# Kernel optimization log

Hardware: AMD Instinct MI355X
Metric: run time of the kernel (lower is better)

## Reference

```python
import jax, jax.numpy as jnp
import numpy as np

MAX_LAB = 64  # cap on connected-component ids per sample (original cc3d is unbounded)
BIG = jnp.int32(2 ** 30)


def _cc_label(mask):
    """26-connectivity connected components of a 3D bool mask via label propagation.
    Each component ends with label == max initial voxel id in it (nonzero), bg = 0."""
    n = mask.size
    init = jnp.where(mask, jnp.arange(1, n + 1, dtype=jnp.int32).reshape(mask.shape), jnp.int32(0))

    def cond(st):
        return jnp.any(st[0] != st[1])

    def body(st):
        lab = st[0]
        # max over 3x3x3 neighborhood == 26-connectivity propagation step
        neigh = jax.lax.reduce_window(lab, jnp.int32(0), jax.lax.max, (3, 3, 3), (1, 1, 1), 'SAME')
        return (jnp.where(mask, neigh, jnp.int32(0)), lab)

    lab, _ = jax.lax.while_loop(cond, body, (init, jnp.full_like(init, -1)))
    return lab


def _compact(lab):
    """Relabel a per-sample label map to consecutive ids 0,1..k (0 = background),
    matching cc3d's 1..k numbering."""
    u = jnp.unique(lab, size=MAX_LAB + 1, fill_value=BIG)  # sorted: [0, l1, .., lk, BIG..]
    return jnp.searchsorted(u, lab).astype(jnp.int32)


def _instance_dice(x, y):
    xb = jnp.squeeze(x, 1) > 0.5  # [B,D,H,W] pred foreground
    yb = jnp.squeeze(y, 1) > 0.5  # [B,D,H,W] gt foreground
    label = jax.vmap(lambda m: _compact(_cc_label(m)))
    gt_lab = label(yb)  # per-sample ids 0..k_i (ids shared across batch, as in original)
    pr_lab = label(xb)
    M = MAX_LAB + 1
    # joint histogram over (gt component id, pred component id), global across batch
    idx = gt_lab.reshape(-1) * M + pr_lab.reshape(-1)
    overlap = jax.ops.segment_sum(jnp.ones(idx.shape, jnp.float32), idx, num_segments=M * M).reshape(M, M)
    gt_size = overlap.sum(1)  # [M] voxels per gt id
    pr_size = overlap.sum(0)  # [M] voxels per pred id
    ov = overlap[1:, 1:]                       # [G,P] fg-fg overlaps
    inter_mask = ov > 0                        # pred comp p intersects gt comp g
    inter = ov.sum(1)                          # [G] |gt_g  ∩  union(intersecting preds)|
    union_sz = (inter_mask * pr_size[1:]).sum(1)  # [G] |union of intersecting pred comps|
    has_inter = inter > 0
    dice = jnp.where(has_inter, 2.0 * inter / jnp.maximum(union_sz + gt_size[1:], 1.0), 0.0)
    lesion_dice = dice.sum()
    num_gt = jnp.sum(gt_size[1:] > 0).astype(jnp.float32)
    tp_mask = inter_mask.any(0)                # [P] pred comps matched to some gt
    num_fp = jnp.sum((pr_size[1:] > 0) & ~tp_mask).astype(jnp.float32)
    return lesion_dice / (num_gt + num_fp)


def setup_inputs() -> dict:
    B, D, H, W = 2, 128, 128, 128
    R, N_BLOBS = 5, 12
    rng = np.random.default_rng(0)
    zz, yy, xx = np.meshgrid(np.arange(D), np.arange(H), np.arange(W), indexing='ij')

    def blobs(k):
        m = np.zeros((B, D, H, W), bool)
        for b in range(B):
            c = rng.integers(R + 2, D - R - 2, size=(k, 3))
            for cz, cy, cx in c:
                m[b] |= (zz - cz) ** 2 + (yy - cy) ** 2 + (xx - cx) ** 2 <= R * R
        return m

    y = blobs(N_BLOBS)
    # prediction = slightly shifted gt (partial-overlap TPs) + extra false-positive blobs
    x = np.roll(y, shift=(2, 1, 0), axis=(1, 2, 3)) | blobs(4)
    return {"x": jnp.asarray(x[:, None].astype(np.float32)),
            "y": jnp.asarray(y[:, None].astype(np.float32))}


def reference(x, y):
    return _instance_dice(x, y)
```

## Files before the change

kernel.cpp:

```cpp
#include <hip/hip_runtime.h>


#define NVOX (128 * 128 * 128)
#define NTOT (2 * NVOX)
#define NBLK 4096
#define CAP 12288
#define ML 65
#define NSLAB 8
#define ZSLAB 16
#define EDGE_CAP 8192
#define OVBLK 48

__global__ __launch_bounds__(256) void k_count(
    const float4* __restrict__ x, const float4* __restrict__ y,
    unsigned char* __restrict__ maskArr, int* __restrict__ blkCnt,
    int* __restrict__ overlap, int* __restrict__ cnt) {
    int t = blockIdx.x * 256 + threadIdx.x;
    float4 xv = x[t];
    float4 yv = y[t];
    unsigned m = 0;
    if (xv.x > 0.5f) m |= 1u;
    if (xv.y > 0.5f) m |= 2u;
    if (xv.z > 0.5f) m |= 4u;
    if (xv.w > 0.5f) m |= 8u;
    if (yv.x > 0.5f) m |= 16u;
    if (yv.y > 0.5f) m |= 32u;
    if (yv.z > 0.5f) m |= 64u;
    if (yv.w > 0.5f) m |= 128u;
    maskArr[t] = (unsigned char)m;
    int v = __popc(m & 0xFu) | (__popc(m >> 4) << 16);
    #pragma unroll
    for (int d = 1; d < 64; d <<= 1) v += __shfl_xor(v, d);
    __shared__ int ws[4];
    if ((threadIdx.x & 63) == 0) ws[threadIdx.x >> 6] = v;
    __syncthreads();
    if (threadIdx.x == 0) blkCnt[blockIdx.x] = ws[0] + ws[1] + ws[2] + ws[3];
    if (blockIdx.x == 0) {
        for (int i = threadIdx.x; i < ML * ML; i += 256) overlap[i] = 0;
        if (threadIdx.x < 8) cnt[8 + threadIdx.x] = 0;
    }
}

__global__ __launch_bounds__(1024) void k_scan(
    const int* __restrict__ blkCnt, int* __restrict__ blkOff, int* __restrict__ cnt) {
    int t = threadIdx.x;
    int base = t * 4;
    int a0 = blkCnt[base], a1 = blkCnt[base + 1], a2 = blkCnt[base + 2], a3 = blkCnt[base + 3];
    int s = a0 + a1 + a2 + a3;
    int lane = t & 63, wave = t >> 6;
    int v = s;
    #pragma unroll
    for (int d = 1; d < 64; d <<= 1) {
        int u = __shfl_up(v, d);
        if (lane >= d) v += u;
    }
    __shared__ int wsum[16];
    __shared__ int segb;
    if (lane == 63) wsum[wave] = v;
    __syncthreads();
    int woff = 0;
    for (int k = 0; k < wave; ++k) woff += wsum[k];
    int incl = v + woff;
    int excl = incl - s;
    if (t == 511) segb = incl;
    __syncthreads();
    int sub = (base >= 2048) ? segb : 0;
    int e0 = excl - sub;
    blkOff[base]     = e0;
    blkOff[base + 1] = e0 + a0;
    blkOff[base + 2] = e0 + a0 + a1;
    blkOff[base + 3] = e0 + a0 + a1 + a2;
    if (t == 511) { cnt[0] = incl & 0xFFFF; cnt[2] = incl >> 16; }
    if (t == 1023) {
        cnt[1] = (incl & 0xFFFF) - (segb & 0xFFFF);
        cnt[3] = (incl >> 16)    - (segb >> 16);
    }
}

__global__ __launch_bounds__(256) void k_fill(
    const unsigned char* __restrict__ maskArr, const int* __restrict__ blkOff,
    unsigned short* __restrict__ posMapX, unsigned short* __restrict__ posMapY,
    int* __restrict__ lists) {
    int blk = blockIdx.x;
    int t = blk * 256 + threadIdx.x;
    int b = blk >> 11;
    unsigned m = maskArr[t];
    int px = __popc(m & 0xFu), py = __popc(m >> 4);
    int pk = px | (py << 16);
    int lane = threadIdx.x & 63, wave = threadIdx.x >> 6;
    int v = pk;
    #pragma unroll
    for (int d = 1; d < 64; d <<= 1) {
        int u = __shfl_up(v, d);
        if (lane >= d) v += u;
    }
    __shared__ int wsum[4];
    if (lane == 63) wsum[wave] = v;
    __syncthreads();
    int woff = 0;
    for (int k = 0; k < wave; ++k) woff += wsum[k];
    int incl = v + woff;
    int off = blkOff[blk];
    int baseX = (off & 0xFFFF) + (incl & 0xFFFF) - px;
    int baseY = (off >> 16)    + (incl >> 16)    - py;
    int i = t << 2;
    int j = i & (NVOX - 1);
    ushort4 pxv, pyv;
    unsigned short* ppx = &pxv.x;
    unsigned short* ppy = &pyv.x;
    int cx = 0, cy = 0;
    #pragma unroll
    for (int k = 0; k < 4; ++k) {
        unsigned short vx = 0, vy = 0;
        if (m & (1u << k)) {
            int pos = baseX + cx++;
            if (pos < CAP) { lists[(0 + b) * CAP + pos] = j + k; vx = (unsigned short)(pos + 1); }
        }
        if (m & (1u << (k + 4))) {
            int pos = baseY + cy++;
            if (pos < CAP) { lists[(2 + b) * CAP + pos] = j + k; vy = (unsigned short)(pos + 1); }
        }
        ppx[k] = vx;
        ppy[k] = vy;
    }
    ((ushort4*)posMapX)[t] = pxv;
    ((ushort4*)posMapY)[t] = pyv;
}

__device__ __forceinline__ int find_root(volatile unsigned* parent, int i) {
    unsigned p = parent[i];
    while (p != (unsigned)i) {
        unsigned gp = parent[p];
        if (gp != p) parent[i] = gp;
        i = (int)p;
        p = gp;
    }
    return i;
}

__device__ __forceinline__ void lds_union(unsigned* parentNV, int a, int b) {
    volatile unsigned* parent = (volatile unsigned*)parentNV;
    int ra = find_root(parent, a);
    int rb = find_root(parent, b);
    while (ra != rb) {
        int lo = ra < rb ? ra : rb;
        int hi = ra < rb ? rb : ra;
        unsigned old = atomicCAS(&parentNV[lo], (unsigned)lo, (unsigned)hi);
        if (old == (unsigned)lo) return;
        ra = find_root(parent, (int)old);
        rb = find_root(parent, hi);
    }
}

__global__ __launch_bounds__(1024) void k_cc_local(
    const unsigned short* __restrict__ posMapX, const unsigned short* __restrict__ posMapY,
    const int* __restrict__ lists, const int* __restrict__ blkOff,
    int* __restrict__ cnt, int* __restrict__ rootPos, int* __restrict__ edges) {
    int fb = blockIdx.y;
    int slab = blockIdx.x;
    int f = fb >> 1, b = fb & 1;
    const unsigned short* posMap = (f ? posMapY : posMapX) + (b << 21);
    const int* fgl = lists + fb * CAP;
    int n = cnt[fb]; if (n > CAP) n = CAP;
    int blkbase = b * 2048 + slab * 256;
    int o0 = blkOff[blkbase];
    int s0 = f ? (o0 >> 16) : (o0 & 0xFFFF);
    int s1;
    if (slab == NSLAB - 1) s1 = n;
    else { int o1 = blkOff[blkbase + 256]; s1 = f ? (o1 >> 16) : (o1 & 0xFFFF); }
    if (s1 > n) s1 = n;
    int ns = s1 - s0;
    if (ns <= 0) return;

    __shared__ unsigned parent[CAP];
    int tid = threadIdx.x;
    int lane = tid & 63;
    int iters = (ns + 1023) >> 10;

    for (int it = 0; it < iters; ++it) {
        int q = it * 1024 + tid;
        if (q < ns) {
            int p = s0 + q;
            int j = fgl[p];
            unsigned par = (unsigned)q;
            if (p + 1 < s1 && (j & 127) != 127) {
                if (fgl[p + 1] == j + 1) par = (unsigned)(q + 1);
            }
            parent[q] = par;
        }
    }
    __syncthreads();

    for (int it = 0; it < iters; ++it) {
        int q = it * 1024 + tid;
        bool active = q < ns;
        int j = active ? fgl[s0 + q] : 0;
        int z = j >> 14, y = (j >> 7) & 127, x0 = j & 127;
        bool ztop = ((z & (ZSLAB - 1)) == (ZSLAB - 1));
        unsigned short qv[12];
        int idx = 0;
        #pragma unroll
        for (int dx = -1; dx <= 1; ++dx) {
            int yy = y + 1, xx = x0 + dx;
            bool ok = active && yy <= 127 && (unsigned)xx <= 127u;
            int nj = (z << 14) + (yy << 7) + xx;
            qv[idx++] = ok ? posMap[nj] : (unsigned short)0;
        }
        #pragma unroll
        for (int dy = -1; dy <= 1; ++dy)
            #pragma unroll
            for (int dx = -1; dx <= 1; ++dx) {
                int zz = z + 1, yy = y + dy, xx = x0 + dx;
                bool ok = active && zz <= 127 && (unsigned)yy <= 127u && (unsigned)xx <= 127u;
                int nj = (zz << 14) + (yy << 7) + xx;
                qv[idx++] = ok ? posMap[nj] : (unsigned short)0;
            }
        #pragma unroll
        for (int k = 0; k < 3; ++k)
            if (qv[k]) lds_union(parent, q, (int)qv[k] - 1 - s0);
        if (!ztop) {
            #pragma unroll
            for (int k = 3; k < 12; ++k)
                if (qv[k]) lds_union(parent, q, (int)qv[k] - 1 - s0);
        }
        int ec = 0;
        int myE[9];
        if (ztop) {
            #pragma unroll
            for (int k = 3; k < 12; ++k)
                if (qv[k]) myE[ec++] = (s0 + q) | (((int)qv[k] - 1) << 14);
        }
        int pref = ec;
        #pragma unroll
        for (int d = 1; d < 64; d <<= 1) {
            int u = __shfl_up(pref, d);
            if (lane >= d) pref += u;
        }
        int total = __shfl(pref, 63);
        if (total > 0) {
            int base = 0;
            if (lane == 63) base = atomicAdd(cnt + 8 + fb, total);
            base = __shfl(base, 63);
            int o = base + pref - ec;
            for (int k = 0; k < ec; ++k)
                if (o + k < EDGE_CAP) edges[fb * EDGE_CAP + o + k] = myE[k];
        }
    }
    __syncthreads();

    for (int it = 0; it < iters; ++it) {
        int q = it * 1024 + tid;
        if (q < ns)
            rootPos[fb * CAP + s0 + q] = s0 + find_root((volatile unsigned*)parent, q);
    }
}

__device__ __forceinline__ int rank_of(const int* sortedL, int nr, int v) {
    int lo = 0, hi = nr;
    while (lo < hi) { int mid = (lo + hi) >> 1; if (sortedL[mid] < v) lo = mid + 1; else hi = mid; }
    return lo;
}

__global__ __launch_bounds__(1024) void k_cc_merge(
    const int* __restrict__ cnt, const int* __restrict__ rootPos,
    const int* __restrict__ edges, unsigned char* __restrict__ lab8) {
    int fb = blockIdx.x;
    int tid = threadIdx.x;
    int n = cnt[fb]; if (n > CAP) n = CAP;
    int ne = cnt[8 + fb]; if (ne > EDGE_CAP) ne = EDGE_CAP;

    __shared__ unsigned parent[CAP];
    __shared__ int slabRoots[1024];
    __shared__ int rootsL[128];
    __shared__ int sortedL[64];
    __shared__ int nsrSh, nrSh;

    if (tid == 0) { nsrSh = 0; nrSh = 0; }
    __syncthreads();
    for (int p = tid; p < n; p += 1024) {
        unsigned r = (unsigned)rootPos[fb * CAP + p];
        parent[p] = r;
        if (r == (unsigned)p) {
            int s = atomicAdd(&nsrSh, 1);
            if (s < 1024) slabRoots[s] = p;
        }
    }
    __syncthreads();

    for (int e = tid; e < ne; e += 1024) {
        int pk = edges[fb * EDGE_CAP + e];
        lds_union(parent, pk & 0x3FFF, pk >> 14);
    }
    __syncthreads();

    int nsr = nsrSh; if (nsr > 1024) nsr = 1024;
    for (int i = tid; i < nsr; i += 1024) {
        int r = slabRoots[i];
        if (parent[r] == (unsigned)r) {
            int s = atomicAdd(&nrSh, 1);
            if (s < 128) rootsL[s] = r;
        }
    }
    __syncthreads();
    int nr = nrSh; if (nr > 64) nr = 64;
    if (tid < nr) {
        int v = rootsL[tid];
        int r = 0;
        for (int k = 0; k < nr; ++k) r += (rootsL[k] < v) ? 1 : 0;
        sortedL[r] = v;
    }
    __syncthreads();

    for (int i = tid; i < nsr; i += 1024) {
        int r = slabRoots[i];
        int fr = find_root((volatile unsigned*)parent, r);
        lab8[fb * CAP + r] = (unsigned char)(1 + rank_of(sortedL, nr, fr));
    }
}

__device__ __forceinline__ void hist_add_pred(int* ovl, int key, bool valid) {
    unsigned long long remaining = __ballot(valid ? 1 : 0);
    int lane = threadIdx.x & 63;
    while (remaining) {
        int leader = __ffsll(remaining) - 1;
        int lkey = __shfl(key, leader);
        unsigned long long m = __ballot((valid && lkey == key) ? 1 : 0) & remaining;
        if (lane == leader) atomicAdd(&ovl[lkey], (int)__popcll(m));
        remaining &= ~m;
    }
}

__global__ __launch_bounds__(256) void k_overlap_final(
    const unsigned short* __restrict__ posMapX, const unsigned short* __restrict__ posMapY,
    const int* __restrict__ lists, int* __restrict__ cnt,
    const int* __restrict__ rootPos, const unsigned char* __restrict__ lab8,
    int* __restrict__ overlap, float* __restrict__ out) {
    int fb = blockIdx.y;
    int f = fb >> 1, b = fb & 1;
    int n = cnt[fb]; if (n > CAP) n = CAP;
    int t = blockIdx.x * 256 + threadIdx.x;
    bool valid = t < n;
    int key = 0;
    if (valid) {
        int j = lists[fb * CAP + t];
        int gi = (b << 21) + j;
        if (f == 0) {
            int pc = (int)lab8[fb * CAP + rootPos[fb * CAP + t]];
            int q = (int)posMapY[gi];
            int gc = 0;
            if (q) gc = (int)lab8[(2 + b) * CAP + rootPos[(2 + b) * CAP + (q - 1)]];
            key = gc * ML + pc;
        } else {
            if (posMapX[gi] != 0) valid = false;
            else {
                int gc = (int)lab8[fb * CAP + rootPos[fb * CAP + t]];
                key = gc * ML;
            }
        }
    }
    hist_add_pred(overlap, key, valid);

    __shared__ int lastFlag;
    __syncthreads();
    if (threadIdx.x == 0) {
        __threadfence();
        lastFlag = (atomicAdd(&cnt[12], 1) == 4 * OVBLK - 1) ? 1 : 0;
    }
    __syncthreads();
    if (!lastFlag) return;

    __shared__ int O[ML * ML];
    __shared__ float prs[ML];
    __shared__ unsigned char tp[ML];
    __shared__ float diceSh[ML];
    __shared__ int ngSh[ML];
    __shared__ int nfSh[ML];
    int tid = threadIdx.x;
    for (int i = tid; i < ML * ML; i += 256) O[i] = overlap[i];
    __syncthreads();
    if (tid < ML) {
        int s = 0; int any = 0;
        for (int g = 0; g < ML; ++g) {
            int o = O[g * ML + tid];
            s += o;
            if (g >= 1 && o > 0) any = 1;
        }
        prs[tid] = (float)s;
        tp[tid] = (unsigned char)any;
    }
    __syncthreads();
    if (tid < ML) {
        float dice = 0.f; int ng = 0, nf = 0;
        if (tid >= 1) {
            int gt = 0, inter = 0; float un = 0.f;
            for (int p = 0; p < ML; ++p) {
                int o = O[tid * ML + p];
                gt += o;
                if (p >= 1) { inter += o; if (o > 0) un += prs[p]; }
            }
            if (inter > 0) {
                float den = un + (float)gt;
                if (den < 1.f) den = 1.f;
                dice = 2.f * (float)inter / den;
            }
            ng = (gt > 0) ? 1 : 0;
            nf = (prs[tid] > 0.f && tp[tid] == 0) ? 1 : 0;
        }
        diceSh[tid] = dice; ngSh[tid] = ng; nfSh[tid] = nf;
    }
    __syncthreads();
    if (tid == 0) {
        float ld = 0.f; int ng = 0, nf = 0;
        for (int k = 1; k < ML; ++k) { ld += diceSh[k]; ng += ngSh[k]; nf += nfSh[k]; }
        out[0] = ld / (float)(ng + nf);
    }
}

extern "C" void kernel_launch(void* const* d_in, const int* in_sizes, int n_in,
                              void* d_out, int out_size, void* d_ws, size_t ws_size,
                              hipStream_t stream) {
    const float* x = (const float*)d_in[0];
    const float* y = (const float*)d_in[1];
    float* out = (float*)d_out;

    char* base = (char*)d_ws;
    int* cnt            = (int*)base;
    int* overlap        = cnt + 16;
    int* blkCnt         = overlap + ML * ML;
    int* blkOff         = blkCnt + NBLK;
    int* lists          = blkOff + NBLK;
    int* rootPos        = lists + 4 * CAP;
    int* edges          = rootPos + 4 * CAP;
    unsigned char* lab8 = (unsigned char*)(edges + 4 * EDGE_CAP);
    unsigned char* maskArr = lab8 + 4 * CAP;
    size_t off = (size_t)((maskArr + NTOT / 4) - (unsigned char*)base);
    off = (off + 15) & ~(size_t)15;
    unsigned short* posMapX = (unsigned short*)(base + off);
    unsigned short* posMapY = posMapX + NTOT;

    k_count<<<NBLK, 256, 0, stream>>>((const float4*)x, (const float4*)y,
                                      maskArr, blkCnt, overlap, cnt);
    k_scan<<<1, 1024, 0, stream>>>(blkCnt, blkOff, cnt);
    k_fill<<<NBLK, 256, 0, stream>>>(maskArr, blkOff, posMapX, posMapY, lists);
    k_cc_local<<<dim3(NSLAB, 4), 1024, 0, stream>>>(posMapX, posMapY, lists,
                                                    blkOff, cnt, rootPos, edges);
    k_cc_merge<<<4, 1024, 0, stream>>>(cnt, rootPos, edges, lab8);
    k_overlap_final<<<dim3(OVBLK, 4), 256, 0, stream>>>(
        posMapX, posMapY, lists, cnt, rootPos, lab8, overlap, out);
}
```

Baseline: 142.9 us.

## Fold block scan into fill and merge CC stage via last-block pattern

Removes the single-block scan kernel: every fill block now reads all 4096 block counts and computes its own prefix offset and the per-sample totals redundantly. The local connected-components kernel and the merge kernel are fused, with the last slab block per (field, batch) pair detected through an atomic counter plus threadfence and then doing the merge. This cuts two kernel launches and their serialization gaps. In exchange every fill block reads 16 KB of counts, and the merge now runs on only the last-arriving block while sharing LDS with the local stage.

```diff
diff --git a/kernel.cpp b/kernel.cpp
--- a/kernel.cpp
+++ b/kernel.cpp
@@ -37,72 +37,75 @@
     if (threadIdx.x == 0) blkCnt[blockIdx.x] = ws[0] + ws[1] + ws[2] + ws[3];
     if (blockIdx.x == 0) {
         for (int i = threadIdx.x; i < ML * ML; i += 256) overlap[i] = 0;
-        if (threadIdx.x < 8) cnt[8 + threadIdx.x] = 0;
-    }
-}
-
-__global__ __launch_bounds__(1024) void k_scan(
-    const int* __restrict__ blkCnt, int* __restrict__ blkOff, int* __restrict__ cnt) {
-    int t = threadIdx.x;
-    int base = t * 4;
-    int a0 = blkCnt[base], a1 = blkCnt[base + 1], a2 = blkCnt[base + 2], a3 = blkCnt[base + 3];
-    int s = a0 + a1 + a2 + a3;
-    int lane = t & 63, wave = t >> 6;
-    int v = s;
+        if (threadIdx.x < 16) cnt[8 + threadIdx.x] = 0;
+    }
+}
+
+__global__ __launch_bounds__(256) void k_fill(
+    const unsigned char* __restrict__ maskArr, const int* __restrict__ blkCnt,
+    int* __restrict__ blkOff, int* __restrict__ cnt,
+    unsigned short* __restrict__ posMapX, unsigned short* __restrict__ posMapY,
+    int* __restrict__ lists) {
+    int blk = blockIdx.x;
+    int tid = threadIdx.x;
+    int lane = tid & 63, wave = tid >> 6;
+
+    int A = 0, B = 0, C = 0;
+    #pragma unroll
+    for (int k = 0; k < 4; ++k) {
+        int4 c4 = ((const int4*)blkCnt)[tid * 4 + k];
+        int i0 = tid * 16 + k * 4;
+        const int* cc = &c4.x;
+        #pragma unroll
+        for (int j = 0; j < 4; ++j) {
+            int c = cc[j];
+            int i = i0 + j;
+            C += c;
+            if (i < 2048) B += c;
+            if (i < blk)  A += c;
+        }
+    }
+    #pragma unroll
+    for (int d = 1; d < 64; d <<= 1) {
+        A += __shfl_xor(A, d);
+        B += __shfl_xor(B, d);
+        C += __shfl_xor(C, d);
+    }
+    __shared__ int rA[4], rB[4], rC[4];
+    if (lane == 0) { rA[wave] = A; rB[wave] = B; rC[wave] = C; }
+    __syncthreads();
+    A = rA[0] + rA[1] + rA[2] + rA[3];
+    B = rB[0] + rB[1] + rB[2] + rB[3];
+    C = rC[0] + rC[1] + rC[2] + rC[3];
+    int base = A - (blk >= 2048 ? B : 0);
+    if (tid == 0) {
+        blkOff[blk] = base;
+        if (blk == 0) {
+            cnt[0] = B & 0xFFFF;
+            cnt[2] = B >> 16;
+            cnt[1] = (C & 0xFFFF) - (B & 0xFFFF);
+            cnt[3] = (C >> 16)    - (B >> 16);
+        }
+    }
+
+    int t = blk * 256 + tid;
+    int b = blk >> 11;
+    unsigned m = maskArr[t];
+    int px = __popc(m & 0xFu), py = __popc(m >> 4);
+    int v = px | (py << 16);
     #pragma unroll
     for (int d = 1; d < 64; d <<= 1) {
         int u = __shfl_up(v, d);
         if (lane >= d) v += u;
     }
-    __shared__ int wsum[16];
-    __shared__ int segb;
+    __shared__ int wsum[4];
     if (lane == 63) wsum[wave] = v;
     __syncthreads();
     int woff = 0;
     for (int k = 0; k < wave; ++k) woff += wsum[k];
     int incl = v + woff;
-    int excl = incl - s;
-    if (t == 511) segb = incl;
-    __syncthreads();
-    int sub = (base >= 2048) ? segb : 0;
-    int e0 = excl - sub;
-    blkOff[base]     = e0;
-    blkOff[base + 1] = e0 + a0;
-    blkOff[base + 2] = e0 + a0 + a1;
-    blkOff[base + 3] = e0 + a0 + a1 + a2;
-    if (t == 511) { cnt[0] = incl & 0xFFFF; cnt[2] = incl >> 16; }
-    if (t == 1023) {
-        cnt[1] = (incl & 0xFFFF) - (segb & 0xFFFF);
-        cnt[3] = (incl >> 16)    - (segb >> 16);
-    }
-}
-
-__global__ __launch_bounds__(256) void k_fill(
-    const unsigned char* __restrict__ maskArr, const int* __restrict__ blkOff,
-    unsigned short* __restrict__ posMapX, unsigned short* __restrict__ posMapY,
-    int* __restrict__ lists) {
-    int blk = blockIdx.x;
-    int t = blk * 256 + threadIdx.x;
-    int b = blk >> 11;
-    unsigned m = maskArr[t];
-    int px = __popc(m & 0xFu), py = __popc(m >> 4);
-    int pk = px | (py << 16);
-    int lane = threadIdx.x & 63, wave = threadIdx.x >> 6;
-    int v = pk;
-    #pragma unroll
-    for (int d = 1; d < 64; d <<= 1) {
-        int u = __shfl_up(v, d);
-        if (lane >= d) v += u;
-    }
-    __shared__ int wsum[4];
-    if (lane == 63) wsum[wave] = v;
-    __syncthreads();
-    int woff = 0;
-    for (int k = 0; k < wave; ++k) woff += wsum[k];
-    int incl = v + woff;
-    int off = blkOff[blk];
-    int baseX = (off & 0xFFFF) + (incl & 0xFFFF) - px;
-    int baseY = (off >> 16)    + (incl >> 16)    - py;
+    int baseX = (base & 0xFFFF) + (incl & 0xFFFF) - px;
+    int baseY = (base >> 16)    + (incl >> 16)    - py;
     int i = t << 2;
     int j = i & (NVOX - 1);
     ushort4 pxv, pyv;
@@ -152,10 +155,17 @@
     }
 }
 
-__global__ __launch_bounds__(1024) void k_cc_local(
+__device__ __forceinline__ int rank_of(const int* sortedL, int nr, int v) {
+    int lo = 0, hi = nr;
+    while (lo < hi) { int mid = (lo + hi) >> 1; if (sortedL[mid] < v) lo = mid + 1; else hi = mid; }
+    return lo;
+}
+
+__global__ __launch_bounds__(1024) void k_cc(
     const unsigned short* __restrict__ posMapX, const unsigned short* __restrict__ posMapY,
     const int* __restrict__ lists, const int* __restrict__ blkOff,
-    int* __restrict__ cnt, int* __restrict__ rootPos, int* __restrict__ edges) {
+    int* __restrict__ cnt, int* __restrict__ rootPos, int* __restrict__ edges,
+    unsigned char* __restrict__ lab8) {
     int fb = blockIdx.y;
     int slab = blockIdx.x;
     int f = fb >> 1, b = fb & 1;
@@ -170,113 +180,109 @@
     else { int o1 = blkOff[blkbase + 256]; s1 = f ? (o1 >> 16) : (o1 & 0xFFFF); }
     if (s1 > n) s1 = n;
     int ns = s1 - s0;
-    if (ns <= 0) return;
-
-    __shared__ unsigned parent[CAP];
-    int tid = threadIdx.x;
-    int lane = tid & 63;
-    int iters = (ns + 1023) >> 10;
-
-    for (int it = 0; it < iters; ++it) {
-        int q = it * 1024 + tid;
-        if (q < ns) {
-            int p = s0 + q;
-            int j = fgl[p];
-            unsigned par = (unsigned)q;
-            if (p + 1 < s1 && (j & 127) != 127) {
-                if (fgl[p + 1] == j + 1) par = (unsigned)(q + 1);
-            }
-            parent[q] = par;
-        }
-    }
-    __syncthreads();
-
-    for (int it = 0; it < iters; ++it) {
-        int q = it * 1024 + tid;
-        bool active = q < ns;
-        int j = active ? fgl[s0 + q] : 0;
-        int z = j >> 14, y = (j >> 7) & 127, x0 = j & 127;
-        bool ztop = ((z & (ZSLAB - 1)) == (ZSLAB - 1));
-        unsigned short qv[12];
-        int idx = 0;
-        #pragma unroll
-        for (int dx = -1; dx <= 1; ++dx) {
-            int yy = y + 1, xx = x0 + dx;
-            bool ok = active && yy <= 127 && (unsigned)xx <= 127u;
-            int nj = (z << 14) + (yy << 7) + xx;
-            qv[idx++] = ok ? posMap[nj] : (unsigned short)0;
-        }
-        #pragma unroll
-        for (int dy = -1; dy <= 1; ++dy)
-            #pragma unroll
-            for (int dx = -1; dx <= 1; ++dx) {
-                int zz = z + 1, yy = y + dy, xx = x0 + dx;
-                bool ok = active && zz <= 127 && (unsigned)yy <= 127u && (unsigned)xx <= 127u;
-                int nj = (zz << 14) + (yy << 7) + xx;
-                qv[idx++] = ok ? posMap[nj] : (unsigned short)0;
-            }
-        #pragma unroll
-        for (int k = 0; k < 3; ++k)
-            if (qv[k]) lds_union(parent, q, (int)qv[k] - 1 - s0);
-        if (!ztop) {
-            #pragma unroll
-            for (int k = 3; k < 12; ++k)
-                if (qv[k]) lds_union(parent, q, (int)qv[k] - 1 - s0);
-        }
-        int ec = 0;
-        int myE[9];
-        if (ztop) {
-            #pragma unroll
-            for (int k = 3; k < 12; ++k)
-                if (qv[k]) myE[ec++] = (s0 + q) | (((int)qv[k] - 1) << 14);
-        }
-        int pref = ec;
-        #pragma unroll
-        for (int d = 1; d < 64; d <<= 1) {
-            int u = __shfl_up(pref, d);
-            if (lane >= d) pref += u;
-        }
-        int total = __shfl(pref, 63);
-        if (total > 0) {
-            int base = 0;
-            if (lane == 63) base = atomicAdd(cnt + 8 + fb, total);
-            base = __shfl(base, 63);
-            int o = base + pref - ec;
-            for (int k = 0; k < ec; ++k)
-                if (o + k < EDGE_CAP) edges[fb * EDGE_CAP + o + k] = myE[k];
-        }
-    }
-    __syncthreads();
-
-    for (int it = 0; it < iters; ++it) {
-        int q = it * 1024 + tid;
-        if (q < ns)
-            rootPos[fb * CAP + s0 + q] = s0 + find_root((volatile unsigned*)parent, q);
-    }
-}
-
-__device__ __forceinline__ int rank_of(const int* sortedL, int nr, int v) {
-    int lo = 0, hi = nr;
-    while (lo < hi) { int mid = (lo + hi) >> 1; if (sortedL[mid] < v) lo = mid + 1; else hi = mid; }
-    return lo;
-}
-
-__global__ __launch_bounds__(1024) void k_cc_merge(
-    const int* __restrict__ cnt, const int* __restrict__ rootPos,
-    const int* __restrict__ edges, unsigned char* __restrict__ lab8) {
-    int fb = blockIdx.x;
-    int tid = threadIdx.x;
-    int n = cnt[fb]; if (n > CAP) n = CAP;
-    int ne = cnt[8 + fb]; if (ne > EDGE_CAP) ne = EDGE_CAP;
 
     __shared__ unsigned parent[CAP];
     __shared__ int slabRoots[1024];
     __shared__ int rootsL[128];
     __shared__ int sortedL[64];
-    __shared__ int nsrSh, nrSh;
-
-    if (tid == 0) { nsrSh = 0; nrSh = 0; }
-    __syncthreads();
+    __shared__ int nsrSh, nrSh, lastFlag;
+    int tid = threadIdx.x;
+    int lane = tid & 63;
+
+    if (ns > 0) {
+        int iters = (ns + 1023) >> 10;
+
+        for (int it = 0; it < iters; ++it) {
+            int q = it * 1024 + tid;
+            if (q < ns) {
+                int p = s0 + q;
+                int j = fgl[p];
+                unsigned par = (unsigned)q;
+                if (p + 1 < s1 && (j & 127) != 127) {
+                    if (fgl[p + 1] == j + 1) par = (unsigned)(q + 1);
+                }
+                parent[q] = par;
+            }
+        }
+        __syncthreads();
+
+        for (int it = 0; it < iters; ++it) {
+            int q = it * 1024 + tid;
+            bool active = q < ns;
+            int j = active ? fgl[s0 + q] : 0;
+            int z = j >> 14, y = (j >> 7) & 127, x0 = j & 127;
+            bool ztop = ((z & (ZSLAB - 1)) == (ZSLAB - 1));
+            unsigned short qv[12];
+            int idx = 0;
+            #pragma unroll
+            for (int dx = -1; dx <= 1; ++dx) {
+                int yy = y + 1, xx = x0 + dx;
+                bool ok = active && yy <= 127 && (unsigned)xx <= 127u;
+                int nj = (z << 14) + (yy << 7) + xx;
+                qv[idx++] = ok ? posMap[nj] : (unsigned short)0;
+            }
+            #pragma unroll
+            for (int dy = -1; dy <= 1; ++dy)
+                #pragma unroll
+                for (int dx = -1; dx <= 1; ++dx) {
+                    int zz = z + 1, yy = y + dy, xx = x0 + dx;
+                    bool ok = active && zz <= 127 && (unsigned)yy <= 127u && (unsigned)xx <= 127u;
+                    int nj = (zz << 14) + (yy << 7) + xx;
+                    qv[idx++] = ok ? posMap[nj] : (unsigned short)0;
+                }
+            #pragma unroll
+            for (int k = 0; k < 3; ++k)
+                if (qv[k]) lds_union(parent, q, (int)qv[k] - 1 - s0);
+            if (!ztop) {
+                #pragma unroll
+                for (int k = 3; k < 12; ++k)
+                    if (qv[k]) lds_union(parent, q, (int)qv[k] - 1 - s0);
+            }
+            int ec = 0;
+            int myE[9];
+            if (ztop) {
+                #pragma unroll
+                for (int k = 3; k < 12; ++k)
+                    if (qv[k]) myE[ec++] = (s0 + q) | (((int)qv[k] - 1) << 14);
+            }
+            int pref = ec;
+            #pragma unroll
+            for (int d = 1; d < 64; d <<= 1) {
+                int u = __shfl_up(pref, d);
+                if (lane >= d) pref += u;
+            }
+            int total = __shfl(pref, 63);
+            if (total > 0) {
+                int ebase = 0;
+                if (lane == 63) ebase = atomicAdd(cnt + 8 + fb, total);
+                ebase = __shfl(ebase, 63);
+                int o = ebase + pref - ec;
+                for (int k = 0; k < ec; ++k)
+                    if (o + k < EDGE_CAP) edges[fb * EDGE_CAP + o + k] = myE[k];
+            }
+        }
+        __syncthreads();
+
+        for (int it = 0; it < iters; ++it) {
+            int q = it * 1024 + tid;
+            if (q < ns)
+                rootPos[fb * CAP + s0 + q] = s0 + find_root((volatile unsigned*)parent, q);
+        }
+    }
+    __syncthreads();
+
+    if (tid == 0) {
+        __threadfence();
+        lastFlag = (atomicAdd(&cnt[16 + fb], 1) == NSLAB - 1) ? 1 : 0;
+        nsrSh = 0; nrSh = 0;
+    }
+    __syncthreads();
+    if (!lastFlag) return;
+    __threadfence();
+
+    int ne = atomicAdd(cnt + 8 + fb, 0);
+    if (ne > EDGE_CAP) ne = EDGE_CAP;
+
     for (int p = tid; p < n; p += 1024) {
         unsigned r = (unsigned)rootPos[fb * CAP + p];
         parent[p] = r;
@@ -425,7 +431,7 @@
 
     char* base = (char*)d_ws;
     int* cnt            = (int*)base;
-    int* overlap        = cnt + 16;
+    int* overlap        = cnt + 32;
     int* blkCnt         = overlap + ML * ML;
     int* blkOff         = blkCnt + NBLK;
     int* lists          = blkOff + NBLK;
@@ -440,11 +446,10 @@
 
     k_count<<<NBLK, 256, 0, stream>>>((const float4*)x, (const float4*)y,
                                       maskArr, blkCnt, overlap, cnt);
-    k_scan<<<1, 1024, 0, stream>>>(blkCnt, blkOff, cnt);
-    k_fill<<<NBLK, 256, 0, stream>>>(maskArr, blkOff, posMapX, posMapY, lists);
-    k_cc_local<<<dim3(NSLAB, 4), 1024, 0, stream>>>(posMapX, posMapY, lists,
-                                                    blkOff, cnt, rootPos, edges);
-    k_cc_merge<<<4, 1024, 0, stream>>>(cnt, rootPos, edges, lab8);
+    k_fill<<<NBLK, 256, 0, stream>>>(maskArr, blkCnt, blkOff, cnt,
+                                     posMapX, posMapY, lists);
+    k_cc<<<dim3(NSLAB, 4), 1024, 0, stream>>>(posMapX, posMapY, lists, blkOff,
+                                              cnt, rootPos, edges, lab8);
     k_overlap_final<<<dim3(OVBLK, 4), 256, 0, stream>>>(
         posMapX, posMapY, lists, cnt, rootPos, lab8, overlap, out);
 }
```

Result: slower. 146.4 us (+2.5%).
